# Optimization experiments

Measured on AMD Instinct MI355X. Metric: run time of the kernel, lower is better.

The kernel has to match this reference:

```python
import jax, jax.numpy as jnp
import numpy as np

B, T, F = 8, 1024, 80
STACK, STRIDE = 4, 4          # encoder.embed.right_context+1, subsampling_rate
G, E, C = 4, 16, 8192         # num_codebooks, embedding_dim, num_embeddings
DENC = 512                    # encoder.output_size()
TS = (T - STACK) // STRIDE + 1
FREG = 0.01                   # features_regularization_weight
EPS = 1e-5


def setup_inputs() -> dict:
    key = jax.random.key(0)
    ks = jax.random.split(key, 12)
    feats = jax.random.normal(ks[0], (B, T, F), jnp.float32)
    feats_lengths = jax.random.randint(ks[1], (B,), T // 2, T + 1, jnp.int32)
    # span masks (True = masked), mask_length=10 spans so full subsample windows get masked
    n_spans, ML = 16, 10
    starts = jax.random.randint(ks[2], (B, n_spans), 0, T - ML)
    pos = starts[:, :, None] + jnp.arange(ML)  # [B, n_spans, ML]
    masks = jnp.zeros((B, T), bool).at[jnp.arange(B)[:, None, None], pos].set(True)
    mask_emb = 0.1 * jax.random.normal(ks[3], (1, 1, F), jnp.float32)
    signal_mean = 0.1 * jax.random.normal(ks[4], (F,), jnp.float32)
    signal_istd = jax.random.uniform(ks[5], (F,), jnp.float32, 0.5, 1.5)
    projection = jax.random.normal(ks[6], (STACK * F, G * E), jnp.float32) * np.sqrt(2.0 / (STACK * F + G * E))
    embeddings = jax.random.normal(ks[7], (C, G, E), jnp.float32)
    encoder_top_n_out = 0.02 * jax.random.normal(ks[8], (G, DENC, C), jnp.float32)
    encoder_top_n_out_bias = jnp.zeros((G, C), jnp.float32)
    encoder_out = jax.random.normal(ks[9], (B, TS, DENC), jnp.float32)
    return {"feats": feats, "feats_lengths": feats_lengths, "masks": masks,
            "mask_emb": mask_emb, "signal_mean": signal_mean, "signal_istd": signal_istd,
            "projection": projection, "embeddings": embeddings,
            "encoder_top_n_out": encoder_top_n_out,
            "encoder_top_n_out_bias": encoder_top_n_out_bias,
            "encoder_out": encoder_out}


def _quantize_codes(latent, codebook):
    # latent: [N, G*E] -> codes [N, G]; codebook: [C, G, E]
    lat = latent.reshape(latent.shape[0], G, E)
    dist = (jnp.sum(lat ** 2, -1, keepdims=True)
            - 2.0 * jnp.einsum('ngd,cgd->ngc', lat, codebook)
            + jnp.sum(codebook ** 2, -1).T[None])  # [N, G, C]
    return jnp.argmin(dist, axis=-1)


def reference(feats, feats_lengths, masks, mask_emb, signal_mean, signal_istd,
              projection, embeddings, encoder_top_n_out, encoder_top_n_out_bias,
              encoder_out):
    # global CMVN
    xs = (feats - signal_mean) * signal_istd  # [B, T, F]
    features_pen = jnp.mean(xs ** 2)
    # masked signal (fed to the delegated encoder in the original; encoder_out stands in)
    _masked_xs = jnp.where(masks[:, :, None], mask_emb, xs)
    # unfold windows
    widx = jnp.arange(TS)[:, None] * STRIDE + jnp.arange(STACK)  # [TS, STACK]
    code_ids_mask = jnp.all(masks[:, widx], axis=2)  # [B, TS] (torch.min over bool window)
    stacked = xs[:, widx].reshape(B, TS, STACK * F)  # _stack_features on unmasked input
    # LayerNorm (no affine)
    mu = jnp.mean(stacked, -1, keepdims=True)
    var = jnp.var(stacked, -1, keepdims=True)
    normed = (stacked - mu) / jnp.sqrt(var + EPS)
    proj = normed @ projection  # [B, TS, G*E]
    target = _quantize_codes(proj.reshape(B * TS, G * E), embeddings).reshape(B, TS, G)
    # encoder output mask after subsampling
    lens_sub = jnp.maximum((feats_lengths - STACK) // STRIDE + 1, 0)
    out_mask = jnp.arange(TS)[None, :] < lens_sub[:, None]
    m = (out_mask & code_ids_mask).astype(jnp.float32)  # [B, TS]
    # big matmul: [B,1,TS,DENC] x [1,G,DENC,C] + bias -> [B,G,TS,C]
    logits = jnp.einsum('btd,gdc->bgtc', encoder_out, encoder_top_n_out) \
             + encoder_top_n_out_bias[None, :, None, :]
    logp = jax.nn.log_softmax(logits, axis=-1).transpose(0, 2, 1, 3)  # [B, TS, G, C]
    per = -jnp.take_along_axis(logp, target[..., None], axis=-1)[..., 0]  # [B, TS, G]
    denom = jnp.sum(m) + 1e-5
    loss = jnp.sum(per * m[:, :, None]) / (denom * G) + FREG * features_pen
    num_codes = jnp.sum(m) * G
    corr = (jnp.argmax(logits, -1).transpose(0, 2, 1) == target)
    codes_acc = jnp.sum(corr * m[:, :, None]) / num_codes
    vals = (target * m[:, :, None].astype(target.dtype)).reshape(-1)
    uniq_num_codes = jnp.zeros((C,), bool).at[vals].set(True).sum()
    return (loss, codes_acc, features_pen, num_codes, uniq_num_codes)
```

## Files before the change

kernel.cpp:

```cpp
#include <hip/hip_runtime.h>
#include <hip/hip_bf16.h>
#include <math.h>
#include <stddef.h>

#define NB 8
#define NT 1024
#define NF 80
#define NSTACK 4
#define NSTRIDE 4
#define NG 4
#define NE 16
#define NC 8192
#define ND 512
#define NTS 256
#define NP (NB*NTS)
#define SFD (NSTACK*NF)
#define FREG 0.01f
#define LNEPS 1e-5f

#define TCC 1024
#define CPT 4
#define PCH 16
#define PB 16

#define ROWS_MAX 2176
#define ROWCH 144
#define MT 9
#define QCH 16
#define QY 16
#define CT 128
#define QS 8
#define STG16 2304

typedef __attribute__((ext_vector_type(8))) short short8;
typedef __attribute__((ext_vector_type(4))) float f32x4;

struct Ws {
  float penSum;
  unsigned int nA;
  unsigned int maskIsInt;
  unsigned int pad1;
  unsigned long long amax[NP*NG];
  float sumExp[NP*NG];
  float tLogit[NP*NG];
  int   targets[NP*NG];
  int   activeList[NP];
  unsigned int bitmap[NC/32];
  unsigned long long aminS[NP*NG*QS];
  float lat[NP][64];
  unsigned short aHiT[(size_t)(ND/8)*ROWS_MAX*8];
  unsigned short aLoT[(size_t)(ND/8)*ROWS_MAX*8];
  float part_se[NG][ROWS_MAX][CT];
  unsigned long long part_mx[NG][ROWS_MAX][CT];
};

__device__ inline unsigned short bf16_rne(float x) {
  unsigned u = __float_as_uint(x);
  unsigned r = u + 0x7FFFu + ((u >> 16) & 1u);
  return (unsigned short)(r >> 16);
}
__device__ inline unsigned fkey_asc(float d) {
  unsigned u = __float_as_uint(d);
  return (u & 0x80000000u) ? ~u : (u | 0x80000000u);
}
__device__ __forceinline__ void gload_lds16(const void* g, void* l) {
  __builtin_amdgcn_global_load_lds(
      (const __attribute__((address_space(1))) void*)g,
      (__attribute__((address_space(3))) void*)l, 16, 0, 0);
}

__global__ __launch_bounds__(256) void k_prologue(
    const float* __restrict__ feats, const float* __restrict__ mean,
    const float* __restrict__ istd, const unsigned char* __restrict__ m8,
    const int* __restrict__ lens, int doClear, Ws* ws) {
  const int tid = threadIdx.x;
  if (doClear) ws->aminS[(size_t)blockIdx.x*256 + tid] = ~0ull;

  const int N4 = NB*NT*NF/4;
  float s = 0.f;
  for (int i = blockIdx.x*256 + tid; i < N4; i += gridDim.x*256) {
    float4 v = reinterpret_cast<const float4*>(feats)[i];
    int f0 = (i*4) % NF;
    float x0 = (v.x - mean[f0+0]) * istd[f0+0];
    float x1 = (v.y - mean[f0+1]) * istd[f0+1];
    float x2 = (v.z - mean[f0+2]) * istd[f0+2];
    float x3 = (v.w - mean[f0+3]) * istd[f0+3];
    s += x0*x0 + x1*x1 + x2*x2 + x3*x3;
  }
  for (int o = 32; o; o >>= 1) s += __shfl_down(s, o);
  __shared__ float pr[4];
  if ((tid & 63) == 0) pr[tid >> 6] = s;
  __syncthreads();
  if (tid == 0) atomicAdd(&ws->penSum, pr[0]+pr[1]+pr[2]+pr[3]);

  if (blockIdx.x < NP/256) {
    __shared__ unsigned flag;
    if (tid == 0) flag = 0;
    __syncthreads();
    unsigned nz = 0;
    int base = tid * 32;
    for (int i = base; i < base + 32; ++i)
      if ((i & 3) && m8[i]) nz = 1;
    if (nz) atomicOr(&flag, 1u);
    __syncthreads();
    bool isInt = (flag == 0);

    int p = blockIdx.x*256 + tid;
    int b = p >> 8, ts = p & (NTS-1);
    int t0 = b*NT + ts*NSTRIDE;
    bool allm;
    if (isInt) {
      const int* m32 = (const int*)m8;
      allm = m32[t0] && m32[t0+1] && m32[t0+2] && m32[t0+3];
    } else {
      allm = m8[t0] && m8[t0+1] && m8[t0+2] && m8[t0+3];
    }
    int ls = (lens[b] - NSTACK)/NSTRIDE + 1;
    if (ls < 0) ls = 0;
    if (allm && ts < ls) {
      unsigned idx = atomicAdd(&ws->nA, 1u);
      ws->activeList[idx] = p;
    }
  }
}

__global__ __launch_bounds__(256) void k_latprep(
    const float* __restrict__ feats, const float* __restrict__ mean,
    const float* __restrict__ istd, const float* __restrict__ projw,
    const float* __restrict__ enc, Ws* ws) {
  int nA = (int)ws->nA;
  int ai = blockIdx.x;
  int limit = ((nA + ROWCH - 1) / ROWCH) * ROWCH;
  int tid = threadIdx.x;

  if (ai >= nA) {
    if (ai < limit && tid < 64) {
      short8 z;
      #pragma unroll
      for (int j = 0; j < 8; ++j) z[j] = 0;
      *reinterpret_cast<short8*>(ws->aHiT + ((size_t)tid*ROWS_MAX + ai)*8) = z;
      *reinterpret_cast<short8*>(ws->aLoT + ((size_t)tid*ROWS_MAX + ai)*8) = z;
    }
    return;
  }

  int p = ws->activeList[ai];
  if (tid < 64) {
    const float* src = enc + (size_t)p*ND + tid*8;
    float4 x0 = *reinterpret_cast<const float4*>(src);
    float4 x1 = *reinterpret_cast<const float4*>(src + 4);
    float xv[8] = {x0.x, x0.y, x0.z, x0.w, x1.x, x1.y, x1.z, x1.w};
    short8 h, l;
    #pragma unroll
    for (int j = 0; j < 8; ++j) {
      unsigned short hi = bf16_rne(xv[j]);
      float rem = xv[j] - __uint_as_float((unsigned)hi << 16);
      h[j] = (short)hi;
      l[j] = (short)bf16_rne(rem);
    }
    *reinterpret_cast<short8*>(ws->aHiT + ((size_t)tid*ROWS_MAX + ai)*8) = h;
    *reinterpret_cast<short8*>(ws->aLoT + ((size_t)tid*ROWS_MAX + ai)*8) = l;
  }

  int b = p >> 8, ts = p & (NTS-1);
  __shared__ float sN[SFD];
  __shared__ float sPart[4*64];
  __shared__ float rS[4], rQ[4];

  for (int j = tid; j < SFD; j += 256) {
    int k = j / NF, f = j - k*NF;
    sN[j] = (feats[((size_t)b*NT + ts*NSTRIDE + k)*NF + f] - mean[f]) * istd[f];
  }
  __syncthreads();
  float s = 0.f, q = 0.f;
  for (int j = tid; j < SFD; j += 256) { float x = sN[j]; s += x; q += x*x; }
  for (int o = 32; o; o >>= 1) { s += __shfl_down(s, o); q += __shfl_down(q, o); }
  if ((tid & 63) == 0) { rS[tid>>6] = s; rQ[tid>>6] = q; }
  __syncthreads();
  float mu  = (rS[0]+rS[1]+rS[2]+rS[3]) * (1.f/SFD);
  float var = (rQ[0]+rQ[1]+rQ[2]+rQ[3]) * (1.f/SFD) - mu*mu;
  float inv = rsqrtf(var + LNEPS);
  for (int j = tid; j < SFD; j += 256) sN[j] = (sN[j]-mu)*inv;
  __syncthreads();
  {
    int j = tid & 63, part = tid >> 6;
    float a = 0.f;
    int i0 = part*80;
    for (int i = i0; i < i0+80; ++i) a = fmaf(sN[i], projw[i*64 + j], a);
    sPart[part*64 + j] = a;
  }
  __syncthreads();
  if (tid < 64)
    ws->lat[ai][tid] = sPart[tid] + sPart[64+tid] + sPart[128+tid] + sPart[192+tid];
}

__global__ __launch_bounds__(256) void k_qdist(const float* __restrict__ emb, Ws* ws) {
  int nA = (int)ws->nA;
  if (nA == 0) return;
  int tid = threadIdx.x;
  int g = tid >> 6, lane = tid & 63;
  int c = blockIdx.x * 64 + lane;
  int per = (nA + QY - 1) / QY;
  int a0 = blockIdx.y * per;
  int a1 = min(nA, a0 + per);
  int slot = blockIdx.x & (QS-1);

  const float4* e4 = reinterpret_cast<const float4*>(emb + ((size_t)c*NG + g)*NE);
  float4 b0 = e4[0], b1 = e4[1], b2 = e4[2], b3 = e4[3];
  float n2 = b0.x*b0.x + b0.y*b0.y + b0.z*b0.z + b0.w*b0.w
           + b1.x*b1.x + b1.y*b1.y + b1.z*b1.z + b1.w*b1.w
           + b2.x*b2.x + b2.y*b2.y + b2.z*b2.z + b2.w*b2.w
           + b3.x*b3.x + b3.y*b3.y + b3.z*b3.z + b3.w*b3.w;

  __shared__ float sL[QCH][64];
  for (int base = a0; base < a1; base += QCH) {
    int cnt = min(QCH, a1 - base);
    __syncthreads();
    for (int i = tid; i < cnt*64; i += 256)
      (&sL[0][0])[i] = (&ws->lat[0][0])[(size_t)(base + (i >> 6))*64 + (i & 63)];
    __syncthreads();
    for (int i = 0; i < cnt; ++i) {
      const float* lp = &sL[i][g*NE];
      float dot = lp[0]*b0.x + lp[1]*b0.y + lp[2]*b0.z + lp[3]*b0.w
                + lp[4]*b1.x + lp[5]*b1.y + lp[6]*b1.z + lp[7]*b1.w
                + lp[8]*b2.x + lp[9]*b2.y + lp[10]*b2.z + lp[11]*b2.w
                + lp[12]*b3.x + lp[13]*b3.y + lp[14]*b3.z + lp[15]*b3.w;
      float d = n2 - 2.f*dot;
      float mv = d; int mc = c;
      #pragma unroll
      for (int off = 32; off; off >>= 1) {
        float ov = __shfl_xor(mv, off);
        int   oc = __shfl_xor(mc, off);
        if (ov < mv || (ov == mv && oc < mc)) { mv = ov; mc = oc; }
      }
      if (lane == 0) {
        unsigned long long key =
            ((unsigned long long)fkey_asc(mv) << 32) | (unsigned)mc;
        atomicMin(&ws->aminS[(size_t)((base + i)*NG + g)*QS + slot], key);
      }
    }
  }
}

__global__ void k_tgt(Ws* ws) {
  int i = blockIdx.x*256 + threadIdx.x;
  int nA = (int)ws->nA;
  if (i < nA*NG) {
    unsigned long long m = ws->aminS[(size_t)i*QS];
    #pragma unroll
    for (int s = 1; s < QS; ++s) {
      unsigned long long v = ws->aminS[(size_t)i*QS + s];
      if (v < m) m = v;
    }
    int c = (int)(unsigned)(m & 0xFFFFFFFFull);
    ws->targets[i] = c;
    atomicOr(&ws->bitmap[c >> 5], 1u << (c & 31));
  }
}

__global__ __launch_bounds__(512, 4) void k_logits_mfma(
    const float* __restrict__ W, const float* __restrict__ bias, Ws* ws) {
  const int nA = (int)ws->nA;
  if (nA == 0) return;
  const int nCh = (nA + ROWCH - 1) / ROWCH;
  const int tid = threadIdx.x;
  const int wave = tid >> 6, lane = tid & 63;
  const int sub = wave & 3, kh = wave >> 2;
  const int g = blockIdx.y;
  const int c0w = blockIdx.x * 64 + sub * 16;
  const int lo16 = lane & 15, hi4 = lane >> 4;
  const int cA = c0w + lo16;
  const int cOut0 = c0w + hi4*4;
  float bv[4];
  #pragma unroll
  for (int v = 0; v < 4; ++v) bv[v] = bias[g*NC + cOut0 + v];

  __shared__ __align__(16) unsigned char smem[45056];
  unsigned short* sB = (unsigned short*)smem;
  f32x4 (*sAcc)[MT][64] = (f32x4 (*)[MT][64])smem;
  float (*sEs)[ROWCH] = (float (*)[ROWCH])(smem + 36864);
  unsigned long long (*sMx)[ROWCH] =
      (unsigned long long (*)[ROWCH])(smem + 36864 + 2560);

  const float* __restrict__ wBase =
      W + (((size_t)g*ND + (size_t)kh*256 + hi4*8)*NC) + cA;

  for (int ch = 0; ch < nCh; ++ch) {
    const int r0 = ch * ROWCH;

    const unsigned short* gsrc[5];
    #pragma unroll
    for (int i = 0; i < 5; ++i) {
      int t = tid + i*512;
      if (t < STG16) {
        int part = t / 144;
        int row  = t - part*144;
        int h4   = part & 3;
        int khh  = (part >> 2) & 1;
        int hilo = part >> 3;
        const unsigned short* base = hilo ? ws->aLoT : ws->aHiT;
        gsrc[i] = base + ((size_t)(khh*32 + h4)*ROWS_MAX + r0 + row)*8;
      } else {
        gsrc[i] = nullptr;
      }
    }

    f32x4 acc[MT];
    #pragma unroll
    for (int mt = 0; mt < MT; ++mt) acc[mt] = (f32x4){0.f, 0.f, 0.f, 0.f};

    #pragma unroll 1
    for (int step = 0; step < 8; ++step) {
      if (step) __syncthreads();
      float wv[8];
      {
        const float* wp = wBase + (size_t)step*32*NC;
        #pragma unroll
        for (int j = 0; j < 8; ++j) wv[j] = wp[(size_t)j*NC];
      }
      const size_t kAdv = (size_t)step*4*ROWS_MAX*8;
      #pragma unroll
      for (int i = 0; i < 5; ++i) {
        int t = tid + i*512;
        if (t < STG16)
          gload_lds16(gsrc[i] + kAdv, sB + (size_t)t*8);
      }
      __syncthreads();

      short8 whi, wlo;
      #pragma unroll
      for (int j = 0; j < 8; ++j) {
        unsigned short h = bf16_rne(wv[j]);
        float rem = wv[j] - __uint_as_float((unsigned)h << 16);
        whi[j] = (short)h;
        wlo[j] = (short)bf16_rne(rem);
      }
      const unsigned short* bp = sB + ((size_t)((kh*4 + hi4)*144 + lo16))*8;
      #pragma unroll
      for (int mt = 0; mt < MT; ++mt) {
        short8 bh = *reinterpret_cast<const short8*>(bp + mt*128);
        short8 bl = *reinterpret_cast<const short8*>(bp + 9216 + mt*128);
        acc[mt] = __builtin_amdgcn_mfma_f32_16x16x32_bf16(whi, bh, acc[mt], 0, 0, 0);
        acc[mt] = __builtin_amdgcn_mfma_f32_16x16x32_bf16(wlo, bh, acc[mt], 0, 0, 0);
        acc[mt] = __builtin_amdgcn_mfma_f32_16x16x32_bf16(whi, bl, acc[mt], 0, 0, 0);
      }
    }
    __syncthreads();

    if (kh == 1) {
      #pragma unroll
      for (int mt = 0; mt < MT; ++mt) sAcc[sub][mt][lane] = acc[mt];
    }
    __syncthreads();

    if (kh == 0) {
      #pragma unroll
      for (int mt = 0; mt < MT; ++mt) {
        f32x4 oth = sAcc[sub][mt][lane];
        const int row = r0 + mt*16 + lo16;
        const int tgt = (row < nA) ? ws->targets[row*NG + g] : -1;
        float lv[4];
        #pragma unroll
        for (int v = 0; v < 4; ++v) lv[v] = (acc[mt][v] + oth[v]) + bv[v];
        #pragma unroll
        for (int v = 0; v < 4; ++v)
          if (tgt == cOut0 + v) ws->tLogit[row*NG + g] = lv[v];
        float es = expf(lv[0]) + expf(lv[1]) + expf(lv[2]) + expf(lv[3]);
        float mv = lv[0]; int mi = cOut0;
        if (lv[1] > mv) { mv = lv[1]; mi = cOut0+1; }
        if (lv[2] > mv) { mv = lv[2]; mi = cOut0+2; }
        if (lv[3] > mv) { mv = lv[3]; mi = cOut0+3; }
        #pragma unroll
        for (int off = 16; off <= 32; off <<= 1) {
          es += __shfl_xor(es, off);
          float ov = __shfl_xor(mv, off);
          int   oi = __shfl_xor(mi, off);
          if (ov > mv || (ov == mv && oi < mi)) { mv = ov; mi = oi; }
        }
        if (hi4 == 0) {
          sEs[sub][mt*16 + lo16] = es;
          unsigned key = __float_as_uint(mv);
          key = (key & 0x80000000u) ? ~key : (key | 0x80000000u);
          sMx[sub][mt*16 + lo16] = ((unsigned long long)key << 32)
                                 | (unsigned long long)(0xFFFFFFFFu - (unsigned)mi);
        }
      }
    }
    __syncthreads();
    if (tid < ROWCH) {
      float e = sEs[0][tid] + sEs[1][tid] + sEs[2][tid] + sEs[3][tid];
      unsigned long long m0 = sMx[0][tid], m1 = sMx[1][tid];
      unsigned long long m2 = sMx[2][tid], m3 = sMx[3][tid];
      unsigned long long ma = m0 > m1 ? m0 : m1;
      unsigned long long mb = m2 > m3 ? m2 : m3;
      unsigned long long mx = ma > mb ? ma : mb;
      int grow = r0 + tid;
      ws->part_se[g][grow][blockIdx.x] = e;
      ws->part_mx[g][grow][blockIdx.x] = mx;
    }
    __syncthreads();
  }
}

__global__ __launch_bounds__(256) void k_red_l(Ws* ws) {
  int nA = (int)ws->nA;
  int pair = blockIdx.x*4 + (threadIdx.x >> 6);
  int lane = threadIdx.x & 63;
  int row = pair >> 2, g = pair & 3;
  if (row >= nA) return;
  float e = ws->part_se[g][row][lane] + ws->part_se[g][row][lane + 64];
  unsigned long long a = ws->part_mx[g][row][lane];
  unsigned long long b = ws->part_mx[g][row][lane + 64];
  unsigned long long mx = a > b ? a : b;
  #pragma unroll
  for (int off = 32; off; off >>= 1) {
    e += __shfl_xor(e, off);
    unsigned long long o = __shfl_xor(mx, off);
    if (o > mx) mx = o;
  }
  if (lane == 0) {
    ws->sumExp[row*NG + g] = e;
    ws->amax[row*NG + g] = mx;
  }
}

__global__ __launch_bounds__(256) void k_quant(
    const float* __restrict__ feats, const float* __restrict__ mean,
    const float* __restrict__ istd, const float* __restrict__ projw,
    const float* __restrict__ emb, Ws* ws) {
  if (blockIdx.x >= ws->nA) return;
  int ai = blockIdx.x;
  int p = ws->activeList[ai];
  int b = p >> 8, ts = p & (NTS-1);
  int tid = threadIdx.x;
  __shared__ float sN[SFD];
  __shared__ float sPart[4*64];
  __shared__ float sLat[NG*NE];
  __shared__ float sRedS[256];
  __shared__ int   sRedC[256];
  __shared__ float rS[4], rQ[4];
  __shared__ int   sTgt[NG];

  for (int j = tid; j < SFD; j += 256) {
    int k = j / NF, f = j - k*NF;
    sN[j] = (feats[((size_t)b*NT + ts*NSTRIDE + k)*NF + f] - mean[f]) * istd[f];
  }
  __syncthreads();
  float s = 0.f, q = 0.f;
  for (int j = tid; j < SFD; j += 256) { float x = sN[j]; s += x; q += x*x; }
  for (int o = 32; o; o >>= 1) { s += __shfl_down(s, o); q += __shfl_down(q, o); }
  if ((tid & 63) == 0) { rS[tid>>6] = s; rQ[tid>>6] = q; }
  __syncthreads();
  float mu  = (rS[0]+rS[1]+rS[2]+rS[3]) * (1.f/SFD);
  float var = (rQ[0]+rQ[1]+rQ[2]+rQ[3]) * (1.f/SFD) - mu*mu;
  float inv = rsqrtf(var + LNEPS);
  for (int j = tid; j < SFD; j += 256) sN[j] = (sN[j]-mu)*inv;
  __syncthreads();
  {
    int j = tid & 63, part = tid >> 6;
    float a = 0.f;
    int i0 = part*80;
    for (int i = i0; i < i0+80; ++i) a = fmaf(sN[i], projw[i*64 + j], a);
    sPart[part*64 + j] = a;
  }
  __syncthreads();
  if (tid < 64) sLat[tid] = sPart[tid] + sPart[64+tid] + sPart[128+tid] + sPart[192+tid];
  __syncthreads();

  for (int gg = 0; gg < NG; ++gg) {
    float lg[NE];
    #pragma unroll
    for (int e = 0; e < NE; ++e) lg[e] = sLat[gg*NE + e];
    float best = 3.4e38f; int bc = NC;
    for (int c = tid; c < NC; c += 256) {
      const float4* cb4 = reinterpret_cast<const float4*>(emb + ((size_t)c*NG + gg)*NE);
      float4 a0 = cb4[0], a1 = cb4[1], a2 = cb4[2], a3 = cb4[3];
      float dot = 0.f, n2 = 0.f;
      dot = fmaf(lg[0],  a0.x, dot); n2 = fmaf(a0.x, a0.x, n2);
      dot = fmaf(lg[1],  a0.y, dot); n2 = fmaf(a0.y, a0.y, n2);
      dot = fmaf(lg[2],  a0.z, dot); n2 = fmaf(a0.z, a0.z, n2);
      dot = fmaf(lg[3],  a0.w, dot); n2 = fmaf(a0.w, a0.w, n2);
      dot = fmaf(lg[4],  a1.x, dot); n2 = fmaf(a1.x, a1.x, n2);
      dot = fmaf(lg[5],  a1.y, dot); n2 = fmaf(a1.y, a1.y, n2);
      dot = fmaf(lg[6],  a1.z, dot); n2 = fmaf(a1.z, a1.z, n2);
      dot = fmaf(lg[7],  a1.w, dot); n2 = fmaf(a1.w, a1.w, n2);
      dot = fmaf(lg[8],  a2.x, dot); n2 = fmaf(a2.x, a2.x, n2);
      dot = fmaf(lg[9],  a2.y, dot); n2 = fmaf(a2.y, a2.y, n2);
      dot = fmaf(lg[10], a2.z, dot); n2 = fmaf(a2.z, a2.z, n2);
      dot = fmaf(lg[11], a2.w, dot); n2 = fmaf(a2.w, a2.w, n2);
      dot = fmaf(lg[12], a3.x, dot); n2 = fmaf(a3.x, a3.x, n2);
      dot = fmaf(lg[13], a3.y, dot); n2 = fmaf(a3.y, a3.y, n2);
      dot = fmaf(lg[14], a3.z, dot); n2 = fmaf(a3.z, a3.z, n2);
      dot = fmaf(lg[15], a3.w, dot); n2 = fmaf(a3.w, a3.w, n2);
      float sc = n2 - 2.f*dot;
      if (sc < best) { best = sc; bc = c; }
    }
    sRedS[tid] = best; sRedC[tid] = bc;
    __syncthreads();
    for (int off = 128; off; off >>= 1) {
      if (tid < off) {
        float os = sRedS[tid+off]; int oc = sRedC[tid+off];
        if (os < sRedS[tid] || (os == sRedS[tid] && oc < sRedC[tid])) {
          sRedS[tid] = os; sRedC[tid] = oc;
        }
      }
      __syncthreads();
    }
    if (tid == 0) sTgt[gg] = sRedC[0];
    __syncthreads();
  }
  if (tid < NG) {
    int c = sTgt[tid];
    ws->targets[ai*NG + tid] = c;
    atomicOr(&ws->bitmap[c >> 5], 1u << (c & 31));
  }
}

__global__ __launch_bounds__(256) void k_logits(
    const float* __restrict__ W, const float* __restrict__ bias,
    const float* __restrict__ enc, Ws* ws) {
  const int nA = (int)ws->nA;
  if (nA == 0) return;
  const int nCh = (nA + PCH - 1) / PCH;
  const int g = blockIdx.y;
  const int cbase = blockIdx.x * TCC + threadIdx.x * CPT;
  const float* __restrict__ Wg = W + (size_t)g*ND*NC;
  const float b0 = bias[g*NC + cbase + 0];
  const float b1 = bias[g*NC + cbase + 1];
  const float b2 = bias[g*NC + cbase + 2];
  const float b3 = bias[g*NC + cbase + 3];
  __shared__ float4 sEnc[PCH][ND/4];
  __shared__ int sP[PCH];

  for (int ch = blockIdx.z; ch < nCh; ch += PB) {
    if (threadIdx.x < PCH) {
      int ai = ch*PCH + threadIdx.x;
      sP[threadIdx.x] = (ai < nA) ? ws->activeList[ai] : -1;
    }
    __syncthreads();
    for (int i = threadIdx.x; i < PCH*(ND/4); i += 256) {
      int qq = i >> 7, r = i & 127;
      int p = sP[qq];
      sEnc[qq][r] = (p >= 0) ? reinterpret_cast<const float4*>(enc)[p*(ND/4) + r]
                             : make_float4(0.f, 0.f, 0.f, 0.f);
    }
    __syncthreads();

    float acc[PCH][CPT];
    #pragma unroll
    for (int qq = 0; qq < PCH; ++qq)
      #pragma unroll
      for (int j = 0; j < CPT; ++j) acc[qq][j] = 0.f;
    for (int d = 0; d < ND; d += 4) {
      const float* wp = Wg + (size_t)d*NC + cbase;
      float4 w0 = *reinterpret_cast<const float4*>(wp);
      float4 w1 = *reinterpret_cast<const float4*>(wp + NC);
      float4 w2 = *reinterpret_cast<const float4*>(wp + 2*NC);
      float4 w3 = *reinterpret_cast<const float4*>(wp + 3*NC);
      int dq = d >> 2;
      #pragma unroll
      for (int qq = 0; qq < PCH; ++qq) {
        float4 e = sEnc[qq][dq];
        acc[qq][0] = fmaf(e.x, w0.x, acc[qq][0]);
        acc[qq][1] = fmaf(e.x, w0.y, acc[qq][1]);
        acc[qq][2] = fmaf(e.x, w0.z, acc[qq][2]);
        acc[qq][3] = fmaf(e.x, w0.w, acc[qq][3]);
        acc[qq][0] = fmaf(e.y, w1.x, acc[qq][0]);
        acc[qq][1] = fmaf(e.y, w1.y, acc[qq][1]);
        acc[qq][2] = fmaf(e.y, w1.z, acc[qq][2]);
        acc[qq][3] = fmaf(e.y, w1.w, acc[qq][3]);
        acc[qq][0] = fmaf(e.z, w2.x, acc[qq][0]);
        acc[qq][1] = fmaf(e.z, w2.y, acc[qq][1]);
        acc[qq][2] = fmaf(e.z, w2.z, acc[qq][2]);
        acc[qq][3] = fmaf(e.z, w2.w, acc[qq][3]);
        acc[qq][0] = fmaf(e.w, w3.x, acc[qq][0]);
        acc[qq][1] = fmaf(e.w, w3.y, acc[qq][1]);
        acc[qq][2] = fmaf(e.w, w3.z, acc[qq][2]);
        acc[qq][3] = fmaf(e.w, w3.w, acc[qq][3]);
      }
    }

    #pragma unroll
    for (int qq = 0; qq < PCH; ++qq) {
      int ai = ch*PCH + qq;
      if (ai < nA) {
        float l0 = acc[qq][0] + b0;
        float l1 = acc[qq][1] + b1;
        float l2 = acc[qq][2] + b2;
        float l3 = acc[qq][3] + b3;
        int tgt = ws->targets[ai*NG + g];
        if ((unsigned)(tgt - cbase) < (unsigned)CPT) {
          float tv = (tgt == cbase) ? l0 : (tgt == cbase+1) ? l1
                   : (tgt == cbase+2) ? l2 : l3;
          ws->tLogit[ai*NG + g] = tv;
        }
        float es = expf(l0) + expf(l1) + expf(l2) + expf(l3);
        float mv = l0; int mi = cbase;
        if (l1 > mv) { mv = l1; mi = cbase+1; }
        if (l2 > mv) { mv = l2; mi = cbase+2; }
        if (l3 > mv) { mv = l3; mi = cbase+3; }
        for (int o = 32; o; o >>= 1) {
          es += __shfl_down(es, o);
          float ov = __shfl_down(mv, o);
          int   oi = __shfl_down(mi, o);
          if (ov > mv || (ov == mv && oi < mi)) { mv = ov; mi = oi; }
        }
        if ((threadIdx.x & 63) == 0) {
          atomicAdd(&ws->sumExp[ai*NG + g], es);
          unsigned key = __float_as_uint(mv);
          key = (key & 0x80000000u) ? ~key : (key | 0x80000000u);
          unsigned long long pk =
              ((unsigned long long)key << 32) |
              (unsigned long long)(0xFFFFFFFFu - (unsigned)mi);
          atomicMax(&ws->amax[ai*NG + g], pk);
        }
      }
    }
    __syncthreads();
  }
}

__global__ __launch_bounds__(256) void k_final(Ws* ws, float* __restrict__ out) {
  int tid = threadIdx.x;
  int nA = (int)ws->nA;
  float sumPer = 0.f, sumCorr = 0.f;
  for (int i = tid; i < nA*NG; i += 256) {
    sumPer += logf(ws->sumExp[i]) - ws->tLogit[i];
    unsigned long long pk = ws->amax[i];
    int mi = (int)(0xFFFFFFFFu - (unsigned)(pk & 0xFFFFFFFFull));
    if (mi == ws->targets[i]) sumCorr += 1.f;
  }
  unsigned w = ws->bitmap[tid];
  if (tid == 0 && nA < NP) w |= 1u;
  int uniq = __popc(w);

  __shared__ float rs[4], rc[4]; __shared__ int ru[4];
  float s1 = sumPer, s2 = sumCorr; int s3 = uniq;
  for (int o = 32; o; o >>= 1) {
    s1 += __shfl_down(s1, o);
    s2 += __shfl_down(s2, o);
    s3 += __shfl_down(s3, o);
  }
  if ((tid & 63) == 0) { rs[tid>>6] = s1; rc[tid>>6] = s2; ru[tid>>6] = s3; }
  __syncthreads();
  if (tid == 0) {
    float sp = rs[0]+rs[1]+rs[2]+rs[3];
    float sc = rc[0]+rc[1]+rc[2]+rc[3];
    int   un = ru[0]+ru[1]+ru[2]+ru[3];
    float pen   = ws->penSum / (float)(NB*NT*NF);
    float denom = (float)nA + 1e-5f;
    float nc    = (float)(nA * NG);
    out[0] = sp / (denom * (float)NG) + FREG * pen;
    out[1] = sc / nc;
    out[2] = pen;
    out[3] = nc;
    out[4] = (float)un;
  }
}

extern "C" void kernel_launch(void* const* d_in, const int* in_sizes, int n_in,
                              void* d_out, int out_size, void* d_ws, size_t ws_size,
                              hipStream_t stream) {
  const float* feats = (const float*)d_in[0];
  const int*   lens  = (const int*)d_in[1];
  const unsigned char* masks = (const unsigned char*)d_in[2];
  const float* mean  = (const float*)d_in[4];
  const float* istd  = (const float*)d_in[5];
  const float* projw = (const float*)d_in[6];
  const float* emb   = (const float*)d_in[7];
  const float* W     = (const float*)d_in[8];
  const float* bias  = (const float*)d_in[9];
  const float* enc   = (const float*)d_in[10];
  Ws* ws = (Ws*)d_ws;
  float* out = (float*)d_out;

  bool big = ws_size >= sizeof(Ws);
  size_t zr = offsetof(Ws, aminS);
  hipMemsetAsync(d_ws, 0, (big || ws_size >= zr) ? zr : ws_size, stream);

  k_prologue<<<256, 256, 0, stream>>>(feats, mean, istd, masks, lens,
                                      big ? 1 : 0, ws);

  if (big) {
    k_latprep<<<ROWS_MAX, 256, 0, stream>>>(feats, mean, istd, projw, enc, ws);
    k_qdist<<<dim3(NC/64, QY), 256, 0, stream>>>(emb, ws);
    k_tgt<<<NP*NG/256, 256, 0, stream>>>(ws);
    k_logits_mfma<<<dim3(CT, NG), 512, 0, stream>>>(W, bias, ws);
    k_red_l<<<NP, 256, 0, stream>>>(ws);
  } else {
    k_quant<<<NP, 256, 0, stream>>>(feats, mean, istd, projw, emb, ws);
    k_logits<<<dim3(NC/TCC, NG, PB), 256, 0, stream>>>(W, bias, enc, ws);
  }
  k_final<<<1, 256, 0, stream>>>(ws, out);
}
```

Baseline: 77.00 us.

## Fuse target selection into MFMA logits kernel and split hi/lo LDS staging

The separate target-reduction kernel is removed: the logits MFMA kernel now reduces the per-slot argmin keys itself, and one block writes the targets. The workspace memset is replaced by a tiny kernel that zeroes only the header. The unique-code bitmap is now built in shared memory inside the final kernel. The MFMA loop stages the hi and lo activation halves in separate LDS buffers, so the next step's hi load overlaps the lo MFMAs. Together these cut launches and memset traffic and overlap staging with compute, at the cost of more barriers per step and relying on k_red_l to overwrite the buffers that are no longer cleared.

```diff
diff --git a/kernel.cpp b/kernel.cpp
--- a/kernel.cpp
+++ b/kernel.cpp
@@ -30,7 +30,7 @@
 #define QY 16
 #define CT 128
 #define QS 8
-#define STG16 2304
+#define STG16H 1152
 
 typedef __attribute__((ext_vector_type(8))) short short8;
 typedef __attribute__((ext_vector_type(4))) float f32x4;
@@ -69,6 +69,15 @@
       (__attribute__((address_space(3))) void*)l, 16, 0, 0);
 }
 
+__global__ void k_zero(Ws* ws) {
+  if (threadIdx.x == 0) {
+    ws->penSum = 0.f;
+    ws->nA = 0u;
+    ws->maskIsInt = 0u;
+    ws->pad1 = 0u;
+  }
+}
+
 __global__ __launch_bounds__(256) void k_prologue(
     const float* __restrict__ feats, const float* __restrict__ mean,
     const float* __restrict__ istd, const unsigned char* __restrict__ m8,
@@ -239,22 +248,6 @@
         atomicMin(&ws->aminS[(size_t)((base + i)*NG + g)*QS + slot], key);
       }
     }
-  }
-}
-
-__global__ void k_tgt(Ws* ws) {
-  int i = blockIdx.x*256 + threadIdx.x;
-  int nA = (int)ws->nA;
-  if (i < nA*NG) {
-    unsigned long long m = ws->aminS[(size_t)i*QS];
-    #pragma unroll
-    for (int s = 1; s < QS; ++s) {
-      unsigned long long v = ws->aminS[(size_t)i*QS + s];
-      if (v < m) m = v;
-    }
-    int c = (int)(unsigned)(m & 0xFFFFFFFFull);
-    ws->targets[i] = c;
-    atomicOr(&ws->bitmap[c >> 5], 1u << (c & 31));
   }
 }
 
@@ -276,7 +269,8 @@
   for (int v = 0; v < 4; ++v) bv[v] = bias[g*NC + cOut0 + v];
 
   __shared__ __align__(16) unsigned char smem[45056];
-  unsigned short* sB = (unsigned short*)smem;
+  unsigned short* sH = (unsigned short*)smem;
+  unsigned short* sLb = (unsigned short*)(smem + 18432);
   f32x4 (*sAcc)[MT][64] = (f32x4 (*)[MT][64])smem;
   float (*sEs)[ROWCH] = (float (*)[ROWCH])(smem + 36864);
   unsigned long long (*sMx)[ROWCH] =
@@ -288,45 +282,41 @@
   for (int ch = 0; ch < nCh; ++ch) {
     const int r0 = ch * ROWCH;
 
-    const unsigned short* gsrc[5];
-    #pragma unroll
-    for (int i = 0; i < 5; ++i) {
-      int t = tid + i*512;
-      if (t < STG16) {
-        int part = t / 144;
-        int row  = t - part*144;
-        int h4   = part & 3;
-        int khh  = (part >> 2) & 1;
-        int hilo = part >> 3;
-        const unsigned short* base = hilo ? ws->aLoT : ws->aHiT;
-        gsrc[i] = base + ((size_t)(khh*32 + h4)*ROWS_MAX + r0 + row)*8;
-      } else {
-        gsrc[i] = nullptr;
-      }
+    size_t off0, off1, off2; bool v2;
+    {
+      int t = tid;
+      int part = t/144, row = t - part*144;
+      off0 = ((size_t)((part>>2)*32 + (part&3))*ROWS_MAX + r0 + row)*8;
+      t = tid + 512;
+      part = t/144; row = t - part*144;
+      off1 = ((size_t)((part>>2)*32 + (part&3))*ROWS_MAX + r0 + row)*8;
+      t = tid + 1024;
+      v2 = (t < STG16H);
+      part = t/144; row = t - part*144;
+      off2 = v2 ? ((size_t)((part>>2)*32 + (part&3))*ROWS_MAX + r0 + row)*8 : 0;
     }
 
     f32x4 acc[MT];
     #pragma unroll
     for (int mt = 0; mt < MT; ++mt) acc[mt] = (f32x4){0.f, 0.f, 0.f, 0.f};
 
+    gload_lds16(ws->aHiT + off0, sH + (size_t)tid*8);
+    gload_lds16(ws->aHiT + off1, sH + (size_t)(tid + 512)*8);
+    if (v2) gload_lds16(ws->aHiT + off2, sH + (size_t)(tid + 1024)*8);
+    __syncthreads();
+
     #pragma unroll 1
     for (int step = 0; step < 8; ++step) {
-      if (step) __syncthreads();
+      const size_t kAdv = (size_t)step*4*ROWS_MAX*8;
+      gload_lds16(ws->aLoT + off0 + kAdv, sLb + (size_t)tid*8);
+      gload_lds16(ws->aLoT + off1 + kAdv, sLb + (size_t)(tid + 512)*8);
+      if (v2) gload_lds16(ws->aLoT + off2 + kAdv, sLb + (size_t)(tid + 1024)*8);
       float wv[8];
       {
         const float* wp = wBase + (size_t)step*32*NC;
         #pragma unroll
         for (int j = 0; j < 8; ++j) wv[j] = wp[(size_t)j*NC];
       }
-      const size_t kAdv = (size_t)step*4*ROWS_MAX*8;
-      #pragma unroll
-      for (int i = 0; i < 5; ++i) {
-        int t = tid + i*512;
-        if (t < STG16)
-          gload_lds16(gsrc[i] + kAdv, sB + (size_t)t*8);
-      }
-      __syncthreads();
-
       short8 whi, wlo;
       #pragma unroll
       for (int j = 0; j < 8; ++j) {
@@ -335,17 +325,28 @@
         whi[j] = (short)h;
         wlo[j] = (short)bf16_rne(rem);
       }
-      const unsigned short* bp = sB + ((size_t)((kh*4 + hi4)*144 + lo16))*8;
+      const unsigned short* bpH = sH + ((size_t)((kh*4 + hi4)*144 + lo16))*8;
       #pragma unroll
       for (int mt = 0; mt < MT; ++mt) {
-        short8 bh = *reinterpret_cast<const short8*>(bp + mt*128);
-        short8 bl = *reinterpret_cast<const short8*>(bp + 9216 + mt*128);
+        short8 bh = *reinterpret_cast<const short8*>(bpH + mt*128);
         acc[mt] = __builtin_amdgcn_mfma_f32_16x16x32_bf16(whi, bh, acc[mt], 0, 0, 0);
         acc[mt] = __builtin_amdgcn_mfma_f32_16x16x32_bf16(wlo, bh, acc[mt], 0, 0, 0);
+      }
+      __syncthreads();
+      if (step < 7) {
+        const size_t kAdv2 = kAdv + (size_t)4*ROWS_MAX*8;
+        gload_lds16(ws->aHiT + off0 + kAdv2, sH + (size_t)tid*8);
+        gload_lds16(ws->aHiT + off1 + kAdv2, sH + (size_t)(tid + 512)*8);
+        if (v2) gload_lds16(ws->aHiT + off2 + kAdv2, sH + (size_t)(tid + 1024)*8);
+      }
+      const unsigned short* bpL = sLb + ((size_t)((kh*4 + hi4)*144 + lo16))*8;
+      #pragma unroll
+      for (int mt = 0; mt < MT; ++mt) {
+        short8 bl = *reinterpret_cast<const short8*>(bpL + mt*128);
         acc[mt] = __builtin_amdgcn_mfma_f32_16x16x32_bf16(whi, bl, acc[mt], 0, 0, 0);
       }
-    }
-    __syncthreads();
+      __syncthreads();
+    }
 
     if (kh == 1) {
       #pragma unroll
@@ -356,9 +357,21 @@
     if (kh == 0) {
       #pragma unroll
       for (int mt = 0; mt < MT; ++mt) {
+        const int row = r0 + mt*16 + lo16;
+        int tgt = -1;
+        if (row < nA) {
+          const unsigned long long* ap = ws->aminS + (size_t)(row*NG + g)*QS;
+          unsigned long long m = ap[0];
+          #pragma unroll
+          for (int s2 = 1; s2 < QS; ++s2) {
+            unsigned long long v = ap[s2];
+            if (v < m) m = v;
+          }
+          tgt = (int)(unsigned)(m & 0xFFFFFFFFull);
+          if (blockIdx.x == 0 && wave == 0 && hi4 == 0)
+            ws->targets[row*NG + g] = tgt;
+        }
         f32x4 oth = sAcc[sub][mt][lane];
-        const int row = r0 + mt*16 + lo16;
-        const int tgt = (row < nA) ? ws->targets[row*NG + g] : -1;
         float lv[4];
         #pragma unroll
         for (int v = 0; v < 4; ++v) lv[v] = (acc[mt][v] + oth[v]) + bv[v];
@@ -509,11 +522,7 @@
     if (tid == 0) sTgt[gg] = sRedC[0];
     __syncthreads();
   }
-  if (tid < NG) {
-    int c = sTgt[tid];
-    ws->targets[ai*NG + tid] = c;
-    atomicOr(&ws->bitmap[c >> 5], 1u << (c & 31));
-  }
+  if (tid < NG) ws->targets[ai*NG + tid] = sTgt[tid];
 }
 
 __global__ __launch_bounds__(256) void k_logits(
@@ -623,14 +632,21 @@
 __global__ __launch_bounds__(256) void k_final(Ws* ws, float* __restrict__ out) {
   int tid = threadIdx.x;
   int nA = (int)ws->nA;
+  __shared__ unsigned sbm[NC/32];
+  sbm[tid] = 0u;
+  __syncthreads();
+
   float sumPer = 0.f, sumCorr = 0.f;
   for (int i = tid; i < nA*NG; i += 256) {
+    int tgt = ws->targets[i];
     sumPer += logf(ws->sumExp[i]) - ws->tLogit[i];
     unsigned long long pk = ws->amax[i];
     int mi = (int)(0xFFFFFFFFu - (unsigned)(pk & 0xFFFFFFFFull));
-    if (mi == ws->targets[i]) sumCorr += 1.f;
-  }
-  unsigned w = ws->bitmap[tid];
+    if (mi == tgt) sumCorr += 1.f;
+    atomicOr(&sbm[tgt >> 5], 1u << (tgt & 31));
+  }
+  __syncthreads();
+  unsigned w = sbm[tid];
   if (tid == 0 && nA < NP) w |= 1u;
   int uniq = __popc(w);
 
@@ -675,19 +691,17 @@
   float* out = (float*)d_out;
 
   bool big = ws_size >= sizeof(Ws);
-  size_t zr = offsetof(Ws, aminS);
-  hipMemsetAsync(d_ws, 0, (big || ws_size >= zr) ? zr : ws_size, stream);
-
-  k_prologue<<<256, 256, 0, stream>>>(feats, mean, istd, masks, lens,
-                                      big ? 1 : 0, ws);
-
   if (big) {
+    k_zero<<<1, 64, 0, stream>>>(ws);
+    k_prologue<<<256, 256, 0, stream>>>(feats, mean, istd, masks, lens, 1, ws);
     k_latprep<<<ROWS_MAX, 256, 0, stream>>>(feats, mean, istd, projw, enc, ws);
     k_qdist<<<dim3(NC/64, QY), 256, 0, stream>>>(emb, ws);
-    k_tgt<<<NP*NG/256, 256, 0, stream>>>(ws);
     k_logits_mfma<<<dim3(CT, NG), 512, 0, stream>>>(W, bias, ws);
     k_red_l<<<NP, 256, 0, stream>>>(ws);
   } else {
+    size_t zr = offsetof(Ws, aminS);
+    hipMemsetAsync(d_ws, 0, ws_size < zr ? ws_size : zr, stream);
+    k_prologue<<<256, 256, 0, stream>>>(feats, mean, istd, masks, lens, 0, ws);
     k_quant<<<NP, 256, 0, stream>>>(feats, mean, istd, projw, emb, ws);
     k_logits<<<dim3(NC/TCC, NG, PB), 256, 0, stream>>>(W, bias, enc, ws);
   }
```

New measurement: 77.64 us. Within noise of the previous version (+0.8%).
